# Performance work log

Hardware: AMD Instinct MI355X
Metric: run time of the kernel (lower is better)

Reference implementation:

```python
import jax, jax.numpy as jnp
import numpy as np

N_AUTHOR, N_PAPER, N_FIELD, N_INST = 100000, 200000, 50000, 8000
IN_F, OUT_F, N_REL = 128, 64, 7


def setup_inputs() -> dict:
    key = jax.random.key(0)
    ks = jax.random.split(key, 24)
    d = {}
    d['x_author'] = jax.random.normal(ks[0], (N_AUTHOR, IN_F), jnp.float32)
    d['x_field_of_study'] = jax.random.normal(ks[1], (N_FIELD, IN_F), jnp.float32)
    d['x_institution'] = jax.random.normal(ks[2], (N_INST, IN_F), jnp.float32)
    d['x_paper'] = jax.random.normal(ks[3], (N_PAPER, IN_F), jnp.float32)
    # params (xavier-ish scale)
    d['weight'] = jax.random.normal(ks[4], (N_REL, IN_F, OUT_F), jnp.float32) * 0.05
    d['self_loop_weight'] = jax.random.normal(ks[5], (IN_F, OUT_F), jnp.float32) * 0.05
    d['bias'] = jnp.zeros((OUT_F,), jnp.float32)
    # edge lists: (name, n_edges, n_src, n_dst)
    rels = [('writes', 1000000, N_AUTHOR, N_PAPER),
            ('rev_writes', 1000000, N_PAPER, N_AUTHOR),
            ('cites', 1000000, N_PAPER, N_PAPER),
            ('has_topic', 800000, N_PAPER, N_FIELD),
            ('rev_has_topic', 800000, N_FIELD, N_PAPER),
            ('affiliated_with', 200000, N_AUTHOR, N_INST),
            ('rev_affiliated_with', 200000, N_INST, N_AUTHOR)]
    i = 6
    for name, ne, ns, nd in rels:
        d[name + '_src'] = jax.random.randint(ks[i], (ne,), 0, ns, jnp.int32); i += 1
        d[name + '_dst'] = jax.random.randint(ks[i], (ne,), 0, nd, jnp.int32); i += 1
    return d


def _rel_conv(x_src, W, src, dst, n_dst):
    # GraphConv(norm='right', weight=W): project src feats (in>out so matmul first),
    # gather along edges, scatter-sum to dst, divide by in-degree (clamped to 1).
    msg = (x_src @ W)[src]                                   # [E, OUT_F]
    agg = jax.ops.segment_sum(msg, dst, num_segments=n_dst)  # [n_dst, OUT_F]
    deg = jax.ops.segment_sum(jnp.ones(dst.shape, msg.dtype), dst, num_segments=n_dst)
    return agg / jnp.maximum(deg, 1.0)[:, None]


def reference(x_author, x_field_of_study, x_institution, x_paper,
              weight, self_loop_weight, bias,
              writes_src, writes_dst, rev_writes_src, rev_writes_dst,
              cites_src, cites_dst, has_topic_src, has_topic_dst,
              rev_has_topic_src, rev_has_topic_dst,
              affiliated_with_src, affiliated_with_dst,
              rev_affiliated_with_src, rev_affiliated_with_dst):
    # weight index order == rel_names order
    h_paper = (_rel_conv(x_author, weight[0], writes_src, writes_dst, N_PAPER)
               + _rel_conv(x_paper, weight[2], cites_src, cites_dst, N_PAPER)
               + _rel_conv(x_field_of_study, weight[4], rev_has_topic_src, rev_has_topic_dst, N_PAPER))
    h_author = (_rel_conv(x_paper, weight[1], rev_writes_src, rev_writes_dst, N_AUTHOR)
                + _rel_conv(x_institution, weight[6], rev_affiliated_with_src, rev_affiliated_with_dst, N_AUTHOR))
    h_field = _rel_conv(x_paper, weight[3], has_topic_src, has_topic_dst, N_FIELD)
    h_inst = _rel_conv(x_author, weight[5], affiliated_with_src, affiliated_with_dst, N_INST)

    def finalize(h, x_dst):
        # self-loop matmul + bias + relu fusion
        return jax.nn.relu(h + x_dst @ self_loop_weight + bias)

    return (finalize(h_author, x_author),
            finalize(h_field, x_field_of_study),
            finalize(h_inst, x_institution),
            finalize(h_paper, x_paper))
```

## Files before the change

### kernel.cpp

```cpp
#include <hip/hip_runtime.h>
#include <hip/hip_bf16.h>

#define IN_F 128
#define OUT_F 64

typedef __hip_bfloat16 bf16;
typedef __attribute__((ext_vector_type(8))) short short8;
typedef __attribute__((ext_vector_type(4))) float f32x4;

#define N_AUTHOR 100000
#define N_PAPER  200000
#define N_FIELD  50000
#define N_INST   8000
#define N_NODES  858000
#define E_TOTAL  5000000

#define OUT_AUTHOR 0L
#define OUT_FIELD  (6400000L)
#define OUT_INST   (9600000L)
#define OUT_PAPER  (10112000L)

#define DG_WRITES   0
#define DG_RWRITES  200000
#define DG_CITES    300000
#define DG_HTOPIC   500000
#define DG_RHTOPIC  550000
#define DG_AFFIL    750000
#define DG_RAFFIL   758000

#define YR_WRITES   0L
#define YR_RWRITES  100000L
#define YR_CITES    300000L
#define YR_HTOPIC   500000L
#define YR_RHTOPIC  700000L
#define YR_AFFIL    750000L
#define YR_RAFFIL   850000L

__device__ inline short f2bf(float f) {
    __hip_bfloat16 h = __float2bfloat16(f);
    return __builtin_bit_cast(short, h);
}
__device__ inline float bflo(unsigned u) {
    unsigned v = u << 16;
    return __builtin_bit_cast(float, v);
}
__device__ inline float bfhi(unsigned u) {
    unsigned v = u & 0xFFFF0000u;
    return __builtin_bit_cast(float, v);
}

__device__ __forceinline__ void degSegS(const int* __restrict__ dst, int E,
                                        int* __restrict__ deg, int chunk,
                                        int lo, int wid) {
    const int base = chunk * 2048 + (int)threadIdx.x * 4;
    #pragma unroll
    for (int it = 0; it < 2; it++) {
        int i = base + it * 1024;
        if (i + 3 < E) {
            int4 d = *(const int4*)(dst + i);
            if ((unsigned)(d.x - lo) < (unsigned)wid) atomicAdd(&deg[d.x], 1);
            if ((unsigned)(d.y - lo) < (unsigned)wid) atomicAdd(&deg[d.y], 1);
            if ((unsigned)(d.z - lo) < (unsigned)wid) atomicAdd(&deg[d.z], 1);
            if ((unsigned)(d.w - lo) < (unsigned)wid) atomicAdd(&deg[d.w], 1);
        } else {
            for (int k = 0; k < 4; k++) {
                int ii = i + k;
                if (ii < E) {
                    int dd = dst[ii];
                    if ((unsigned)(dd - lo) < (unsigned)wid) atomicAdd(&deg[dd], 1);
                }
            }
        }
    }
}

__global__ __launch_bounds__(256) void deg_all(
    const int* d0, const int* d1, const int* d2, const int* d3,
    const int* d4, const int* d5, const int* d6, int* __restrict__ deg) {
    const int b = blockIdx.x;
    const int s = b & 7;
    const int t = b >> 3;
    if      (t < 489)  degSegS(d0, 1000000, deg + DG_WRITES,  t,        s * 25000, 25000);
    else if (t < 978)  degSegS(d1, 1000000, deg + DG_RWRITES, t - 489,  s * 12500, 12500);
    else if (t < 1467) degSegS(d2, 1000000, deg + DG_CITES,   t - 978,  s * 25000, 25000);
    else if (t < 1858) degSegS(d3,  800000, deg + DG_HTOPIC,  t - 1467, s * 6250,  6250);
    else if (t < 2249) degSegS(d4,  800000, deg + DG_RHTOPIC, t - 1858, s * 25000, 25000);
    else if (t < 2347) degSegS(d5,  200000, deg + DG_AFFIL,   t - 2249, s * 1000,  1000);
    else               degSegS(d6,  200000, deg + DG_RAFFIL,  t - 2347, s * 12500, 12500);
}

__global__ __launch_bounds__(256) void scan1(const int* __restrict__ deg,
                                             int* __restrict__ off,
                                             int* __restrict__ bsums, int n) {
    __shared__ int ts[256];
    const int tid = threadIdx.x;
    const int base = blockIdx.x * 1024 + tid * 4;
    int4 v = {0, 0, 0, 0};
    if (base < n) v = *(const int4*)(deg + base);
    int sum = v.x + v.y + v.z + v.w;
    ts[tid] = sum;
    __syncthreads();
    for (int o = 1; o < 256; o <<= 1) {
        int t = (tid >= o) ? ts[tid - o] : 0;
        __syncthreads();
        ts[tid] += t;
        __syncthreads();
    }
    int pre = ts[tid] - sum;
    if (base < n) {
        int4 e;
        e.x = pre;
        e.y = pre + v.x;
        e.z = pre + v.x + v.y;
        e.w = pre + v.x + v.y + v.z;
        *(int4*)(off + base) = e;
    }
    if (tid == 255) bsums[blockIdx.x] = ts[255];
}

__global__ __launch_bounds__(1024) void scan2(int* __restrict__ bsums, int nb) {
    __shared__ int ts[1024];
    const int tid = threadIdx.x;
    int v = (tid < nb) ? bsums[tid] : 0;
    ts[tid] = v;
    __syncthreads();
    for (int o = 1; o < 1024; o <<= 1) {
        int t = (tid >= o) ? ts[tid - o] : 0;
        __syncthreads();
        ts[tid] += t;
        __syncthreads();
    }
    if (tid < nb) bsums[tid] = ts[tid] - v;
}

__global__ __launch_bounds__(256) void scan3(int* __restrict__ off,
                                             int* __restrict__ cursor,
                                             const int* __restrict__ bsums,
                                             int n, int e_total) {
    const int tid = threadIdx.x;
    const int base = blockIdx.x * 1024 + tid * 4;
    const int bp = bsums[blockIdx.x];
    if (base < n) {
        int4 v = *(const int4*)(off + base);
        v.x += bp; v.y += bp; v.z += bp; v.w += bp;
        *(int4*)(off + base) = v;
        *(int4*)(cursor + base) = v;
    }
    if (blockIdx.x == 0 && tid == 0) off[n] = e_total;
}

__device__ __forceinline__ void fillSegS(const int* __restrict__ src,
                                         const int* __restrict__ dst, int E,
                                         int* __restrict__ cursor,
                                         int* __restrict__ csr, int chunk,
                                         int lo, int wid) {
    const int base = chunk * 2048 + (int)threadIdx.x * 4;
    #pragma unroll
    for (int it = 0; it < 2; it++) {
        int i = base + it * 1024;
        if (i + 3 < E) {
            int4 d = *(const int4*)(dst + i);
            int4 sv = *(const int4*)(src + i);
            if ((unsigned)(d.x - lo) < (unsigned)wid) { int p = atomicAdd(&cursor[d.x], 1); csr[p] = sv.x; }
            if ((unsigned)(d.y - lo) < (unsigned)wid) { int p = atomicAdd(&cursor[d.y], 1); csr[p] = sv.y; }
            if ((unsigned)(d.z - lo) < (unsigned)wid) { int p = atomicAdd(&cursor[d.z], 1); csr[p] = sv.z; }
            if ((unsigned)(d.w - lo) < (unsigned)wid) { int p = atomicAdd(&cursor[d.w], 1); csr[p] = sv.w; }
        } else {
            for (int k = 0; k < 4; k++) {
                int ii = i + k;
                if (ii < E) {
                    int dd = dst[ii];
                    if ((unsigned)(dd - lo) < (unsigned)wid) {
                        int p = atomicAdd(&cursor[dd], 1);
                        csr[p] = src[ii];
                    }
                }
            }
        }
    }
}

__global__ __launch_bounds__(256) void fill_all(
    const int* s0, const int* d0, const int* s1, const int* d1,
    const int* s2, const int* d2, const int* s3, const int* d3,
    const int* s4, const int* d4, const int* s5, const int* d5,
    const int* s6, const int* d6,
    int* __restrict__ cursor, int* __restrict__ csr) {
    const int b = blockIdx.x;
    const int s = b & 7;
    const int t = b >> 3;
    if      (t < 489)  fillSegS(s0, d0, 1000000, cursor + DG_WRITES,  csr, t,        s * 25000, 25000);
    else if (t < 978)  fillSegS(s1, d1, 1000000, cursor + DG_RWRITES, csr, t - 489,  s * 12500, 12500);
    else if (t < 1467) fillSegS(s2, d2, 1000000, cursor + DG_CITES,   csr, t - 978,  s * 25000, 25000);
    else if (t < 1858) fillSegS(s3, d3,  800000, cursor + DG_HTOPIC,  csr, t - 1467, s * 6250,  6250);
    else if (t < 2249) fillSegS(s4, d4,  800000, cursor + DG_RHTOPIC, csr, t - 1858, s * 25000, 25000);
    else if (t < 2347) fillSegS(s5, d5,  200000, cursor + DG_AFFIL,   csr, t - 2249, s * 1000,  1000);
    else               fillSegS(s6, d6,  200000, cursor + DG_RAFFIL,  csr, t - 2347, s * 12500, 12500);
}

__global__ __launch_bounds__(256) void prep_wt(const float* __restrict__ W7,
                                               const float* __restrict__ slw,
                                               short* __restrict__ Wt) {
    const int mat = blockIdx.x;
    const float* Ws = (mat < 7) ? (W7 + (size_t)mat * IN_F * OUT_F) : slw;
    short* Wo = Wt + (size_t)mat * IN_F * OUT_F;
    for (int i = threadIdx.x; i < IN_F * OUT_F; i += 256) {
        int n = i >> 7;
        int k = i & 127;
        Wo[i] = f2bf(Ws[k * OUT_F + n]);
    }
}

template <int R>
__device__ __forceinline__ void projBody(
    int blk, int nrows, const float* __restrict__ X,
    const short* __restrict__ wt0, const short* __restrict__ wt1,
    const short* __restrict__ wt2, const short* __restrict__ wtS,
    const float* __restrict__ bias,
    bf16* __restrict__ Y0, bf16* __restrict__ Y1, bf16* __restrict__ Y2,
    float* __restrict__ OutSelf) {
    const int tid = threadIdx.x;
    const int wave = tid >> 6;
    const int lane = tid & 63;
    const int m = lane & 15;
    const int quad = lane >> 4;
    const int rowBase = blk * 64 + wave * 16;
    if (rowBase >= nrows) return;
    const bool full = (rowBase + 16 <= nrows);

    int arow = rowBase + m;
    if (arow > nrows - 1) arow = nrows - 1;

    short8 af[4];
    const float* xrow = X + (size_t)arow * IN_F + quad * 8;
    #pragma unroll
    for (int kb = 0; kb < 4; kb++) {
        float4 x0 = *(const float4*)(xrow + kb * 32);
        float4 x1 = *(const float4*)(xrow + kb * 32 + 4);
        short8 a;
        a[0] = f2bf(x0.x); a[1] = f2bf(x0.y); a[2] = f2bf(x0.z); a[3] = f2bf(x0.w);
        a[4] = f2bf(x1.x); a[5] = f2bf(x1.y); a[6] = f2bf(x1.z); a[7] = f2bf(x1.w);
        af[kb] = a;
    }

    const short* wts[3] = {wt0, wt1, wt2};
    bf16* Ys[3] = {Y0, Y1, Y2};

    #pragma unroll
    for (int r = 0; r < R; r++) {
        bf16* Yr = Ys[r];
        #pragma unroll
        for (int cb = 0; cb < 4; cb++) {
            const int ncol = cb * 16 + m;
            const short* wrow = wts[r] + (size_t)ncol * IN_F + quad * 8;
            f32x4 acc = {0.f, 0.f, 0.f, 0.f};
            #pragma unroll
            for (int kb = 0; kb < 4; kb++) {
                short8 bfr = *(const short8*)(wrow + kb * 32);
                acc = __builtin_amdgcn_mfma_f32_16x16x32_bf16(af[kb], bfr, acc, 0, 0, 0);
            }
            if (full) {
                #pragma unroll
                for (int reg = 0; reg < 4; reg++) {
                    int row = rowBase + quad * 4 + reg;
                    Yr[(size_t)row * OUT_F + ncol] = __float2bfloat16(acc[reg]);
                }
            } else {
                #pragma unroll
                for (int reg = 0; reg < 4; reg++) {
                    int row = rowBase + quad * 4 + reg;
                    if (row < nrows)
                        Yr[(size_t)row * OUT_F + ncol] = __float2bfloat16(acc[reg]);
                }
            }
        }
    }

    #pragma unroll
    for (int cb = 0; cb < 4; cb++) {
        const int ncol = cb * 16 + m;
        const short* wrow = wtS + (size_t)ncol * IN_F + quad * 8;
        f32x4 acc = {0.f, 0.f, 0.f, 0.f};
        #pragma unroll
        for (int kb = 0; kb < 4; kb++) {
            short8 bfr = *(const short8*)(wrow + kb * 32);
            acc = __builtin_amdgcn_mfma_f32_16x16x32_bf16(af[kb], bfr, acc, 0, 0, 0);
        }
        const float b = bias[ncol];
        if (full) {
            #pragma unroll
            for (int reg = 0; reg < 4; reg++) {
                int row = rowBase + quad * 4 + reg;
                OutSelf[(size_t)row * OUT_F + ncol] = acc[reg] + b;
            }
        } else {
            #pragma unroll
            for (int reg = 0; reg < 4; reg++) {
                int row = rowBase + quad * 4 + reg;
                if (row < nrows)
                    OutSelf[(size_t)row * OUT_F + ncol] = acc[reg] + b;
            }
        }
    }
}

__global__ __launch_bounds__(256) void proj_all(
    const float* __restrict__ x_author, const float* __restrict__ x_field,
    const float* __restrict__ x_inst,   const float* __restrict__ x_paper,
    const short* __restrict__ wt, const float* __restrict__ bias,
    bf16* __restrict__ y, float* __restrict__ out) {
    int b = blockIdx.x;
    if (b < 3125) {
        projBody<3>(b, N_PAPER, x_paper, wt + 1 * 8192, wt + 2 * 8192, wt + 3 * 8192, wt + 7 * 8192,
                    bias, y + YR_RWRITES * OUT_F, y + YR_CITES * OUT_F, y + YR_HTOPIC * OUT_F,
                    out + OUT_PAPER);
    } else if (b < 4688) {
        projBody<2>(b - 3125, N_AUTHOR, x_author, wt + 0 * 8192, wt + 5 * 8192, nullptr, wt + 7 * 8192,
                    bias, y + YR_WRITES * OUT_F, y + YR_AFFIL * OUT_F, nullptr,
                    out + OUT_AUTHOR);
    } else if (b < 5470) {
        projBody<1>(b - 4688, N_FIELD, x_field, wt + 4 * 8192, nullptr, nullptr, wt + 7 * 8192,
                    bias, y + YR_RHTOPIC * OUT_F, nullptr, nullptr,
                    out + OUT_FIELD);
    } else {
        projBody<1>(b - 5470, N_INST, x_inst, wt + 6 * 8192, nullptr, nullptr, wt + 7 * 8192,
                    bias, y + YR_RAFFIL * OUT_F, nullptr, nullptr,
                    out + OUT_INST);
    }
}

#define ACC8(racc, u, mk)                                                    \
    racc[0] += mk * bflo(u.x); racc[1] += mk * bfhi(u.x);                    \
    racc[2] += mk * bflo(u.y); racc[3] += mk * bfhi(u.y);                    \
    racc[4] += mk * bflo(u.z); racc[5] += mk * bfhi(u.z);                    \
    racc[6] += mk * bflo(u.w); racc[7] += mk * bfhi(u.w);

template <int NR>
__device__ __forceinline__ void gatherPair(
    int n0, int lane, const char* __restrict__ csrb,
    const int* __restrict__ off0, const char* __restrict__ y0,
    const int* __restrict__ off1, const char* __restrict__ y1,
    const int* __restrict__ off2, const char* __restrict__ y2,
    float* __restrict__ out) {
    const int g = lane >> 3;
    const int f = lane & 7;
    const unsigned foff = (unsigned)f << 4;
    const int* offs[3] = {off0, off1, off2};
    const char* ys[3] = {y0, y1, y2};

    int S[2][NR], E[2][NR];
    #pragma unroll
    for (int r = 0; r < NR; r++) {
        int a = offs[r][n0];
        int b = offs[r][n0 + 1];
        int c = offs[r][n0 + 2];
        S[0][r] = a; E[0][r] = b;
        S[1][r] = b; E[1][r] = c;
    }

    int C[2][NR];
    #pragma unroll
    for (int p = 0; p < 2; p++) {
        #pragma unroll
        for (int r = 0; r < NR; r++) {
            int i = S[p][r] + g;
            int ic = min(i, E[p][r] - 1);
            ic = (S[p][r] < E[p][r]) ? ic : 0;
            C[p][r] = *(const int*)(csrb + ((unsigned)ic << 2));
        }
    }

    uint4 U[2][NR];
    #pragma unroll
    for (int p = 0; p < 2; p++) {
        #pragma unroll
        for (int r = 0; r < NR; r++) {
            U[p][r] = *(const uint4*)(ys[r] + ((unsigned)C[p][r] << 7) + foff);
        }
    }

    float acc[2][8];
    #pragma unroll
    for (int p = 0; p < 2; p++)
        #pragma unroll
        for (int k = 0; k < 8; k++) acc[p][k] = 0.f;

    #pragma unroll
    for (int p = 0; p < 2; p++) {
        #pragma unroll
        for (int r = 0; r < NR; r++) {
            const int s = S[p][r];
            const int e = E[p][r];
            float racc[8] = {0.f, 0.f, 0.f, 0.f, 0.f, 0.f, 0.f, 0.f};
            {
                float mk = (s + g < e) ? 1.f : 0.f;
                uint4 u = U[p][r];
                ACC8(racc, u, mk)
            }
            const char* __restrict__ yb = ys[r];
            for (int j = s + 8; j < e; j += 8) {
                int i = j + g;
                int ic = min(i, e - 1);
                int c2 = *(const int*)(csrb + ((unsigned)ic << 2));
                uint4 u2 = *(const uint4*)(yb + ((unsigned)c2 << 7) + foff);
                float m2 = (i < e) ? 1.f : 0.f;
                ACC8(racc, u2, m2)
            }
            float dg = (float)(e - s);
            float inv = __builtin_amdgcn_rcpf(dg > 1.f ? dg : 1.f);
            #pragma unroll
            for (int k = 0; k < 8; k++) acc[p][k] += racc[k] * inv;
        }
    }

    #pragma unroll
    for (int d = 8; d <= 32; d <<= 1) {
        #pragma unroll
        for (int p = 0; p < 2; p++)
            #pragma unroll
            for (int k = 0; k < 8; k++) acc[p][k] += __shfl_xor(acc[p][k], d, 64);
    }

    if (lane < 8) {
        #pragma unroll
        for (int p = 0; p < 2; p++) {
            float* orow = out + (size_t)(n0 + p) * OUT_F + f * 8;
            float4 c0 = *(float4*)orow;
            float4 c1 = *(float4*)(orow + 4);
            c0.x = fmaxf(c0.x + acc[p][0], 0.f); c0.y = fmaxf(c0.y + acc[p][1], 0.f);
            c0.z = fmaxf(c0.z + acc[p][2], 0.f); c0.w = fmaxf(c0.w + acc[p][3], 0.f);
            c1.x = fmaxf(c1.x + acc[p][4], 0.f); c1.y = fmaxf(c1.y + acc[p][5], 0.f);
            c1.z = fmaxf(c1.z + acc[p][6], 0.f); c1.w = fmaxf(c1.w + acc[p][7], 0.f);
            *(float4*)orow = c0;
            *(float4*)(orow + 4) = c1;
        }
    }
}

__global__ __launch_bounds__(256) void gather_all(
    const int* __restrict__ csr, const int* __restrict__ off,
    const bf16* __restrict__ y, float* __restrict__ out) {
    const int b = blockIdx.x;
    const int tid = threadIdx.x;
    const int lane = tid & 63;
    const int wv = tid >> 6;
    const char* csrb = (const char*)csr;
    if (b < 25000) {
        gatherPair<3>(b * 8 + wv * 2, lane, csrb,
                      off + DG_WRITES,  (const char*)(y + YR_WRITES * OUT_F),
                      off + DG_CITES,   (const char*)(y + YR_CITES * OUT_F),
                      off + DG_RHTOPIC, (const char*)(y + YR_RHTOPIC * OUT_F),
                      out + OUT_PAPER);
    } else if (b < 37500) {
        gatherPair<2>((b - 25000) * 8 + wv * 2, lane, csrb,
                      off + DG_RWRITES, (const char*)(y + YR_RWRITES * OUT_F),
                      off + DG_RAFFIL,  (const char*)(y + YR_RAFFIL * OUT_F),
                      nullptr, nullptr,
                      out + OUT_AUTHOR);
    } else if (b < 43750) {
        gatherPair<1>((b - 37500) * 8 + wv * 2, lane, csrb,
                      off + DG_HTOPIC, (const char*)(y + YR_HTOPIC * OUT_F),
                      nullptr, nullptr, nullptr, nullptr,
                      out + OUT_FIELD);
    } else {
        gatherPair<1>((b - 43750) * 8 + wv * 2, lane, csrb,
                      off + DG_AFFIL, (const char*)(y + YR_AFFIL * OUT_F),
                      nullptr, nullptr, nullptr, nullptr,
                      out + OUT_INST);
    }
}

extern "C" void kernel_launch(void* const* d_in, const int* in_sizes, int n_in,
                              void* d_out, int out_size, void* d_ws, size_t ws_size,
                              hipStream_t stream) {
    (void)in_sizes; (void)n_in; (void)ws_size; (void)out_size;

    const float* x_author = (const float*)d_in[0];
    const float* x_field  = (const float*)d_in[1];
    const float* x_inst   = (const float*)d_in[2];
    const float* x_paper  = (const float*)d_in[3];
    const float* weight   = (const float*)d_in[4];
    const float* slw      = (const float*)d_in[5];
    const float* bias     = (const float*)d_in[6];
    float* out = (float*)d_out;

    char* w = (char*)d_ws;
    auto alignup = [](size_t v) { return (v + 127) & ~(size_t)127; };
    bf16* y  = (bf16*)w;              size_t o1 = alignup((size_t)N_NODES * OUT_F * sizeof(bf16));
    int* deg = (int*)(w + o1);        size_t o2 = o1 + alignup((size_t)N_NODES * sizeof(int));
    int* off = (int*)(w + o2);        size_t o3 = o2 + alignup(((size_t)N_NODES + 4) * sizeof(int));
    int* cursor = (int*)(w + o3);     size_t o4 = o3 + alignup((size_t)N_NODES * sizeof(int));
    int* csr = (int*)(w + o4);        size_t o5 = o4 + alignup((size_t)E_TOTAL * sizeof(int));
    int* bsums = (int*)(w + o5);      size_t o6 = o5 + alignup(2048 * sizeof(int));
    short* wt = (short*)(w + o6);

    const int* ws_p[7] = {(const int*)d_in[7],  (const int*)d_in[9],  (const int*)d_in[11],
                          (const int*)d_in[13], (const int*)d_in[15], (const int*)d_in[17],
                          (const int*)d_in[19]};
    const int* wd_p[7] = {(const int*)d_in[8],  (const int*)d_in[10], (const int*)d_in[12],
                          (const int*)d_in[14], (const int*)d_in[16], (const int*)d_in[18],
                          (const int*)d_in[20]};

    const int NBLK = (N_NODES + 1023) / 1024;
    const int SLICE_BLKS = 8 * 2445;

    prep_wt<<<8, 256, 0, stream>>>(weight, slw, wt);

    hipMemsetAsync(deg, 0, (size_t)N_NODES * sizeof(int), stream);
    deg_all<<<SLICE_BLKS, 256, 0, stream>>>(wd_p[0], wd_p[1], wd_p[2], wd_p[3],
                                            wd_p[4], wd_p[5], wd_p[6], deg);

    scan1<<<NBLK, 256, 0, stream>>>(deg, off, bsums, N_NODES);
    scan2<<<1, 1024, 0, stream>>>(bsums, NBLK);
    scan3<<<NBLK, 256, 0, stream>>>(off, cursor, bsums, N_NODES, E_TOTAL);

    fill_all<<<SLICE_BLKS, 256, 0, stream>>>(ws_p[0], wd_p[0], ws_p[1], wd_p[1],
                                             ws_p[2], wd_p[2], ws_p[3], wd_p[3],
                                             ws_p[4], wd_p[4], ws_p[5], wd_p[5],
                                             ws_p[6], wd_p[6], cursor, csr);

    proj_all<<<5595, 256, 0, stream>>>(x_author, x_field, x_inst, x_paper,
                                       wt, bias, y, out);

    gather_all<<<44750, 256, 0, stream>>>(csr, off, y, out);
}
```

Baseline: 1.007 ms.

## Build degree histogram and CSR fill with per-block LDS destination windows

Replaces the global-atomic degree count and CSR fill with kernels in which each block owns a window of 16384 destination nodes. Each block keeps that window's counters (or cursors) in shared memory and streams the entire edge list of its relation, doing atomics only in LDS. This removes the deg memset, the cursor array and the global atomic traffic, and degrees are written out with plain stores. The cost is only 58 blocks, each rereading a full edge list, which leaves most CUs idle and depends on L2 reuse of the repeated reads.

Result: slower. 1.922 ms (+90.8%).

```diff
diff --git a/kernel.cpp b/kernel.cpp
--- a/kernel.cpp
+++ b/kernel.cpp
@@ -36,6 +36,8 @@
 #define YR_AFFIL    750000L
 #define YR_RAFFIL   850000L
 
+#define WIN 16384
+
 __device__ inline short f2bf(float f) {
     __hip_bfloat16 h = __float2bfloat16(f);
     return __builtin_bit_cast(short, h);
@@ -49,44 +51,42 @@
     return __builtin_bit_cast(float, v);
 }
 
-__device__ __forceinline__ void degSegS(const int* __restrict__ dst, int E,
-                                        int* __restrict__ deg, int chunk,
-                                        int lo, int wid) {
-    const int base = chunk * 2048 + (int)threadIdx.x * 4;
-    #pragma unroll
-    for (int it = 0; it < 2; it++) {
-        int i = base + it * 1024;
-        if (i + 3 < E) {
-            int4 d = *(const int4*)(dst + i);
-            if ((unsigned)(d.x - lo) < (unsigned)wid) atomicAdd(&deg[d.x], 1);
-            if ((unsigned)(d.y - lo) < (unsigned)wid) atomicAdd(&deg[d.y], 1);
-            if ((unsigned)(d.z - lo) < (unsigned)wid) atomicAdd(&deg[d.z], 1);
-            if ((unsigned)(d.w - lo) < (unsigned)wid) atomicAdd(&deg[d.w], 1);
-        } else {
-            for (int k = 0; k < 4; k++) {
-                int ii = i + k;
-                if (ii < E) {
-                    int dd = dst[ii];
-                    if ((unsigned)(dd - lo) < (unsigned)wid) atomicAdd(&deg[dd], 1);
-                }
-            }
-        }
-    }
-}
-
-__global__ __launch_bounds__(256) void deg_all(
+__global__ __launch_bounds__(256) void deg_win(
     const int* d0, const int* d1, const int* d2, const int* d3,
     const int* d4, const int* d5, const int* d6, int* __restrict__ deg) {
+    __shared__ alignas(16) int hist[WIN];
     const int b = blockIdx.x;
-    const int s = b & 7;
-    const int t = b >> 3;
-    if      (t < 489)  degSegS(d0, 1000000, deg + DG_WRITES,  t,        s * 25000, 25000);
-    else if (t < 978)  degSegS(d1, 1000000, deg + DG_RWRITES, t - 489,  s * 12500, 12500);
-    else if (t < 1467) degSegS(d2, 1000000, deg + DG_CITES,   t - 978,  s * 25000, 25000);
-    else if (t < 1858) degSegS(d3,  800000, deg + DG_HTOPIC,  t - 1467, s * 6250,  6250);
-    else if (t < 2249) degSegS(d4,  800000, deg + DG_RHTOPIC, t - 1858, s * 25000, 25000);
-    else if (t < 2347) degSegS(d5,  200000, deg + DG_AFFIL,   t - 2249, s * 1000,  1000);
-    else               degSegS(d6,  200000, deg + DG_RAFFIL,  t - 2347, s * 12500, 12500);
+    const int tid = threadIdx.x;
+    const int* dst; int E, base, nd, win;
+    if      (b < 13) { dst = d0; E = 1000000; base = DG_WRITES;  nd = 200000; win = b; }
+    else if (b < 20) { dst = d1; E = 1000000; base = DG_RWRITES; nd = 100000; win = b - 13; }
+    else if (b < 33) { dst = d2; E = 1000000; base = DG_CITES;   nd = 200000; win = b - 20; }
+    else if (b < 37) { dst = d3; E =  800000; base = DG_HTOPIC;  nd =  50000; win = b - 33; }
+    else if (b < 50) { dst = d4; E =  800000; base = DG_RHTOPIC; nd = 200000; win = b - 37; }
+    else if (b < 51) { dst = d5; E =  200000; base = DG_AFFIL;   nd =   8000; win = b - 50; }
+    else             { dst = d6; E =  200000; base = DG_RAFFIL;  nd = 100000; win = b - 51; }
+    const int lo = win * WIN;
+    int wid = nd - lo; if (wid > WIN) wid = WIN;
+
+    for (int i = tid * 4; i < WIN; i += 1024) {
+        int4 z = {0, 0, 0, 0};
+        *(int4*)(hist + i) = z;
+    }
+    __syncthreads();
+
+    for (int i = tid * 4; i < E; i += 1024) {
+        int4 d = *(const int4*)(dst + i);
+        unsigned a;
+        a = (unsigned)(d.x - lo); if (a < (unsigned)wid) atomicAdd(&hist[a], 1);
+        a = (unsigned)(d.y - lo); if (a < (unsigned)wid) atomicAdd(&hist[a], 1);
+        a = (unsigned)(d.z - lo); if (a < (unsigned)wid) atomicAdd(&hist[a], 1);
+        a = (unsigned)(d.w - lo); if (a < (unsigned)wid) atomicAdd(&hist[a], 1);
+    }
+    __syncthreads();
+
+    int* dout = deg + base + lo;
+    for (int i = tid * 4; i < wid; i += 1024)
+        *(int4*)(dout + i) = *(const int4*)(hist + i);
 }
 
 __global__ __launch_bounds__(256) void scan1(const int* __restrict__ deg,
@@ -134,7 +134,6 @@
 }
 
 __global__ __launch_bounds__(256) void scan3(int* __restrict__ off,
-                                             int* __restrict__ cursor,
                                              const int* __restrict__ bsums,
                                              int n, int e_total) {
     const int tid = threadIdx.x;
@@ -144,58 +143,44 @@
         int4 v = *(const int4*)(off + base);
         v.x += bp; v.y += bp; v.z += bp; v.w += bp;
         *(int4*)(off + base) = v;
-        *(int4*)(cursor + base) = v;
     }
     if (blockIdx.x == 0 && tid == 0) off[n] = e_total;
 }
 
-__device__ __forceinline__ void fillSegS(const int* __restrict__ src,
-                                         const int* __restrict__ dst, int E,
-                                         int* __restrict__ cursor,
-                                         int* __restrict__ csr, int chunk,
-                                         int lo, int wid) {
-    const int base = chunk * 2048 + (int)threadIdx.x * 4;
-    #pragma unroll
-    for (int it = 0; it < 2; it++) {
-        int i = base + it * 1024;
-        if (i + 3 < E) {
-            int4 d = *(const int4*)(dst + i);
-            int4 sv = *(const int4*)(src + i);
-            if ((unsigned)(d.x - lo) < (unsigned)wid) { int p = atomicAdd(&cursor[d.x], 1); csr[p] = sv.x; }
-            if ((unsigned)(d.y - lo) < (unsigned)wid) { int p = atomicAdd(&cursor[d.y], 1); csr[p] = sv.y; }
-            if ((unsigned)(d.z - lo) < (unsigned)wid) { int p = atomicAdd(&cursor[d.z], 1); csr[p] = sv.z; }
-            if ((unsigned)(d.w - lo) < (unsigned)wid) { int p = atomicAdd(&cursor[d.w], 1); csr[p] = sv.w; }
-        } else {
-            for (int k = 0; k < 4; k++) {
-                int ii = i + k;
-                if (ii < E) {
-                    int dd = dst[ii];
-                    if ((unsigned)(dd - lo) < (unsigned)wid) {
-                        int p = atomicAdd(&cursor[dd], 1);
-                        csr[p] = src[ii];
-                    }
-                }
-            }
-        }
-    }
-}
-
-__global__ __launch_bounds__(256) void fill_all(
+__global__ __launch_bounds__(256) void fill_win(
     const int* s0, const int* d0, const int* s1, const int* d1,
     const int* s2, const int* d2, const int* s3, const int* d3,
     const int* s4, const int* d4, const int* s5, const int* d5,
     const int* s6, const int* d6,
-    int* __restrict__ cursor, int* __restrict__ csr) {
+    const int* __restrict__ off, int* __restrict__ csr) {
+    __shared__ alignas(16) int cur[WIN];
     const int b = blockIdx.x;
-    const int s = b & 7;
-    const int t = b >> 3;
-    if      (t < 489)  fillSegS(s0, d0, 1000000, cursor + DG_WRITES,  csr, t,        s * 25000, 25000);
-    else if (t < 978)  fillSegS(s1, d1, 1000000, cursor + DG_RWRITES, csr, t - 489,  s * 12500, 12500);
-    else if (t < 1467) fillSegS(s2, d2, 1000000, cursor + DG_CITES,   csr, t - 978,  s * 25000, 25000);
-    else if (t < 1858) fillSegS(s3, d3,  800000, cursor + DG_HTOPIC,  csr, t - 1467, s * 6250,  6250);
-    else if (t < 2249) fillSegS(s4, d4,  800000, cursor + DG_RHTOPIC, csr, t - 1858, s * 25000, 25000);
-    else if (t < 2347) fillSegS(s5, d5,  200000, cursor + DG_AFFIL,   csr, t - 2249, s * 1000,  1000);
-    else               fillSegS(s6, d6,  200000, cursor + DG_RAFFIL,  csr, t - 2347, s * 12500, 12500);
+    const int tid = threadIdx.x;
+    const int *src, *dst; int E, base, nd, win;
+    if      (b < 13) { src = s0; dst = d0; E = 1000000; base = DG_WRITES;  nd = 200000; win = b; }
+    else if (b < 20) { src = s1; dst = d1; E = 1000000; base = DG_RWRITES; nd = 100000; win = b - 13; }
+    else if (b < 33) { src = s2; dst = d2; E = 1000000; base = DG_CITES;   nd = 200000; win = b - 20; }
+    else if (b < 37) { src = s3; dst = d3; E =  800000; base = DG_HTOPIC;  nd =  50000; win = b - 33; }
+    else if (b < 50) { src = s4; dst = d4; E =  800000; base = DG_RHTOPIC; nd = 200000; win = b - 37; }
+    else if (b < 51) { src = s5; dst = d5; E =  200000; base = DG_AFFIL;   nd =   8000; win = b - 50; }
+    else             { src = s6; dst = d6; E =  200000; base = DG_RAFFIL;  nd = 100000; win = b - 51; }
+    const int lo = win * WIN;
+    int wid = nd - lo; if (wid > WIN) wid = WIN;
+
+    const int* oin = off + base + lo;
+    for (int i = tid * 4; i < wid; i += 1024)
+        *(int4*)(cur + i) = *(const int4*)(oin + i);
+    __syncthreads();
+
+    for (int i = tid * 4; i < E; i += 1024) {
+        int4 d = *(const int4*)(dst + i);
+        int4 sv = *(const int4*)(src + i);
+        unsigned a;
+        a = (unsigned)(d.x - lo); if (a < (unsigned)wid) { int p = atomicAdd(&cur[a], 1); csr[p] = sv.x; }
+        a = (unsigned)(d.y - lo); if (a < (unsigned)wid) { int p = atomicAdd(&cur[a], 1); csr[p] = sv.y; }
+        a = (unsigned)(d.z - lo); if (a < (unsigned)wid) { int p = atomicAdd(&cur[a], 1); csr[p] = sv.z; }
+        a = (unsigned)(d.w - lo); if (a < (unsigned)wid) { int p = atomicAdd(&cur[a], 1); csr[p] = sv.w; }
+    }
 }
 
 __global__ __launch_bounds__(256) void prep_wt(const float* __restrict__ W7,
@@ -493,6 +478,7 @@
     int* csr = (int*)(w + o4);        size_t o5 = o4 + alignup((size_t)E_TOTAL * sizeof(int));
     int* bsums = (int*)(w + o5);      size_t o6 = o5 + alignup(2048 * sizeof(int));
     short* wt = (short*)(w + o6);
+    (void)cursor;
 
     const int* ws_p[7] = {(const int*)d_in[7],  (const int*)d_in[9],  (const int*)d_in[11],
                           (const int*)d_in[13], (const int*)d_in[15], (const int*)d_in[17],
@@ -502,22 +488,20 @@
                           (const int*)d_in[20]};
 
     const int NBLK = (N_NODES + 1023) / 1024;
-    const int SLICE_BLKS = 8 * 2445;
 
     prep_wt<<<8, 256, 0, stream>>>(weight, slw, wt);
 
-    hipMemsetAsync(deg, 0, (size_t)N_NODES * sizeof(int), stream);
-    deg_all<<<SLICE_BLKS, 256, 0, stream>>>(wd_p[0], wd_p[1], wd_p[2], wd_p[3],
-                                            wd_p[4], wd_p[5], wd_p[6], deg);
+    deg_win<<<58, 256, 0, stream>>>(wd_p[0], wd_p[1], wd_p[2], wd_p[3],
+                                    wd_p[4], wd_p[5], wd_p[6], deg);
 
     scan1<<<NBLK, 256, 0, stream>>>(deg, off, bsums, N_NODES);
     scan2<<<1, 1024, 0, stream>>>(bsums, NBLK);
-    scan3<<<NBLK, 256, 0, stream>>>(off, cursor, bsums, N_NODES, E_TOTAL);
-
-    fill_all<<<SLICE_BLKS, 256, 0, stream>>>(ws_p[0], wd_p[0], ws_p[1], wd_p[1],
-                                             ws_p[2], wd_p[2], ws_p[3], wd_p[3],
-                                             ws_p[4], wd_p[4], ws_p[5], wd_p[5],
-                                             ws_p[6], wd_p[6], cursor, csr);
+    scan3<<<NBLK, 256, 0, stream>>>(off, bsums, N_NODES, E_TOTAL);
+
+    fill_win<<<58, 256, 0, stream>>>(ws_p[0], wd_p[0], ws_p[1], wd_p[1],
+                                     ws_p[2], wd_p[2], ws_p[3], wd_p[3],
+                                     ws_p[4], wd_p[4], ws_p[5], wd_p[5],
+                                     ws_p[6], wd_p[6], off, csr);
 
     proj_all<<<5595, 256, 0, stream>>>(x_author, x_field, x_inst, x_paper,
                                        wt, bias, y, out);
```
